# Optimization experiments

Measured on AMD Instinct MI355X. Metric: run time of the kernel, lower is better.

Reference implementation:

```python
import jax, jax.numpy as jnp
import numpy as np

NEG_FILL = -1.0e9
PROB_MIN = 1e-9


def _lstm_cell(x, h, c, w_ih, w_hh, b_ih, b_hh):
    # PyTorch gate order: input, forget, cell(g), output
    gates = x @ w_ih.T + h @ w_hh.T + b_ih + b_hh
    i, f, g, o = jnp.split(gates, 4, axis=-1)
    c_new = jax.nn.sigmoid(f) * c + jax.nn.sigmoid(i) * jnp.tanh(g)
    h_new = jax.nn.sigmoid(o) * jnp.tanh(c_new)
    return h_new, c_new


def setup_inputs() -> dict:
    key = jax.random.key(0)
    B, T, D, H, W = 2048, 100, 128, 256, 256
    ks = jax.random.split(key, 16)
    s_d = 1.0 / np.sqrt(D)
    s_h = 1.0 / np.sqrt(H)
    s_w = 1.0 / np.sqrt(W)
    return {
        "targets": jax.random.normal(ks[0], (B, T, D), jnp.float32),
        "h0": jax.random.normal(ks[1], (1, B, H), jnp.float32),
        "c0": jax.random.normal(ks[2], (1, B, H), jnp.float32),
        "enc_w_ih": jax.random.normal(ks[3], (4 * H, D), jnp.float32) * s_d,
        "enc_w_hh": jax.random.normal(ks[4], (4 * H, H), jnp.float32) * s_h,
        "enc_b_ih": jax.random.normal(ks[5], (4 * H,), jnp.float32) * s_h,
        "enc_b_hh": jax.random.normal(ks[6], (4 * H,), jnp.float32) * s_h,
        "dec_w_ih": jax.random.normal(ks[7], (4 * H, D), jnp.float32) * s_d,
        "dec_w_hh": jax.random.normal(ks[8], (4 * H, H), jnp.float32) * s_h,
        "dec_b_ih": jax.random.normal(ks[9], (4 * H,), jnp.float32) * s_h,
        "dec_b_hh": jax.random.normal(ks[10], (4 * H,), jnp.float32) * s_h,
        "W1": jax.random.normal(ks[11], (W, H), jnp.float32) * s_h,
        "W2": jax.random.normal(ks[12], (W, H), jnp.float32) * s_h,
        "vt": jax.random.normal(ks[13], (W,), jnp.float32) * s_w,
    }


def reference(targets, h0, c0, enc_w_ih, enc_w_hh, enc_b_ih, enc_b_hh,
              dec_w_ih, dec_w_hh, dec_b_ih, dec_b_hh, W1, W2, vt):
    B, T, D = targets.shape
    H = enc_w_hh.shape[1]

    # ---- encoder LSTM (batch_first, zero initial state) ----
    def enc_step(carry, x_t):
        h, c = carry
        h, c = _lstm_cell(x_t, h, c, enc_w_ih, enc_w_hh, enc_b_ih, enc_b_hh)
        return (h, c), h

    z = jnp.zeros((B, H), targets.dtype)
    _, enc_h = jax.lax.scan(enc_step, (z, z), jnp.swapaxes(targets, 0, 1))
    encoder_states = jnp.swapaxes(enc_h, 0, 1)  # [B, T, H]

    blend1 = encoder_states @ W1.T  # [B, T, W]

    a1 = jnp.arange(B)
    init = (h0[0], c0[0], jnp.zeros((B, T), dtype=bool), jnp.zeros_like(targets[:, 0]))

    def dec_step(carry, _):
        h, c, selected, dec_in = carry
        h, c = _lstm_cell(dec_in, h, c, dec_w_ih, dec_w_hh, dec_b_ih, dec_b_hh)
        blend2 = h @ W2.T                                   # [B, W]
        scores = jnp.tanh(blend1 + blend2[:, None, :]) @ vt  # [B, T]
        scores = jnp.where(selected, NEG_FILL, scores)
        sel = jnp.argmax(scores, axis=-1)                    # [B]
        selected = selected.at[a1, sel].set(True)
        probs = jnp.maximum(jax.nn.softmax(scores, axis=-1), PROB_MIN)
        dec_in = targets[a1, sel]                            # [B, D]
        return (h, c, selected, dec_in), probs

    _, probs = jax.lax.scan(dec_step, init, None, length=T)
    return jnp.swapaxes(probs, 0, 1)  # [B, T, T]
```

## Files before the change

### kernel.cpp

```cpp
#include <hip/hip_runtime.h>
#include <math.h>

#define BB   2048
#define TT   100
#define DD   128
#define HH   256
#define NEGF -1.0e9f

__device__ __forceinline__ float sigmoidf_(float x){ return 1.0f/(1.0f+expf(-x)); }

__device__ __forceinline__ float tanh_fast(float x){
  x = fminf(15.f, fmaxf(-15.f, x));
  const float e = __expf(x + x);
  return (e - 1.f) * __builtin_amdgcn_rcpf(e + 1.f);
}

__global__ __launch_bounds__(256) void k_zero_i32(int* __restrict__ p, int n){
  int i = blockIdx.x*256 + threadIdx.x;
  if(i < n) p[i] = 0;
}

__global__ __launch_bounds__(128) void k_gates_cell(
    const float* __restrict__ Xp, int ldx,
    const float* __restrict__ Hp,
    const float* __restrict__ Wih, const float* __restrict__ Whh,
    const float* __restrict__ bih, const float* __restrict__ bhh,
    const float* __restrict__ Cp,
    float* __restrict__ Hout, float* __restrict__ Cout,
    float* __restrict__ Hcopy, int hstride)
{
  __shared__ alignas(16) float Xs[32*68];
  __shared__ alignas(16) float Ws[32*68];
  const int tid = threadIdx.x;
  const int tx = tid & 15;
  const int ty = tid >> 4;
  const int j0 = blockIdx.x * 16;
  const int m0 = blockIdx.y * 64;

  float acc[8][4];
  #pragma unroll
  for(int i=0;i<8;i++)
    #pragma unroll
    for(int s=0;s<4;s++) acc[i][s] = 0.f;

  for(int phase=0; phase<2; phase++){
    const float* Am; int lda; const float* Wm; int ldw; int nt;
    if(phase==0){ if(!Xp) continue; Am=Xp; lda=ldx; Wm=Wih; ldw=DD; nt=4; }
    else        { if(!Hp) continue; Am=Hp; lda=HH;  Wm=Whh; ldw=HH; nt=8; }
    for(int kt=0; kt<nt; kt++){
      const int k0 = kt*32;
      #pragma unroll
      for(int it=0; it<4; it++){
        int q = it*128 + tid; int m = q>>3; int kq = (q&7)<<2;
        const float4 v = *(const float4*)(Am + (size_t)(m0+m)*lda + k0 + kq);
        Xs[(kq+0)*68+m]=v.x; Xs[(kq+1)*68+m]=v.y; Xs[(kq+2)*68+m]=v.z; Xs[(kq+3)*68+m]=v.w;
      }
      #pragma unroll
      for(int it=0; it<4; it++){
        int q = it*128 + tid; int c = q>>3; int kq = (q&7)<<2;
        int n = (c&3)*HH + j0 + (c>>2);
        const float4 v = *(const float4*)(Wm + (size_t)n*ldw + k0 + kq);
        Ws[(kq+0)*68+c]=v.x; Ws[(kq+1)*68+c]=v.y; Ws[(kq+2)*68+c]=v.z; Ws[(kq+3)*68+c]=v.w;
      }
      __syncthreads();
      #pragma unroll
      for(int kk=0; kk<32; kk++){
        const float4 a0 = *(const float4*)&Xs[kk*68 + ty*8];
        const float4 a1 = *(const float4*)&Xs[kk*68 + ty*8 + 4];
        const float4 bv = *(const float4*)&Ws[kk*68 + tx*4];
        const float a[8] = {a0.x,a0.y,a0.z,a0.w,a1.x,a1.y,a1.z,a1.w};
        const float g[4] = {bv.x,bv.y,bv.z,bv.w};
        #pragma unroll
        for(int i=0;i<8;i++)
          #pragma unroll
          for(int s=0;s<4;s++)
            acc[i][s] = fmaf(a[i], g[s], acc[i][s]);
      }
      __syncthreads();
    }
  }

  const int col = j0 + tx;
  const float bi0 = bih[       col] + bhh[       col];
  const float bf0 = bih[  HH + col] + bhh[  HH + col];
  const float bg0 = bih[2*HH + col] + bhh[2*HH + col];
  const float bo0 = bih[3*HH + col] + bhh[3*HH + col];
  #pragma unroll
  for(int i=0;i<8;i++){
    const int b = m0 + ty*8 + i;
    const size_t idx = (size_t)b*HH + col;
    const float iv = acc[i][0] + bi0;
    const float fv = acc[i][1] + bf0;
    const float gv = acc[i][2] + bg0;
    const float ov = acc[i][3] + bo0;
    const float cp = Cp ? Cp[idx] : 0.f;
    const float cn = sigmoidf_(fv)*cp + sigmoidf_(iv)*tanhf(gv);
    const float hn = sigmoidf_(ov)*tanhf(cn);
    Cout[idx] = cn;
    Hout[idx] = hn;
    if(Hcopy) Hcopy[(size_t)b*hstride + col] = hn;
  }
}

__global__ __launch_bounds__(256) void k_gemm_nt(
    const float* __restrict__ A, int lda,
    const float* __restrict__ Bm, int ldb,
    float* __restrict__ C, int ldc, int K)
{
  __shared__ alignas(16) float Xs[32*68];
  __shared__ alignas(16) float Ws[32*68];
  const int tid = threadIdx.x;
  const int tx = tid & 15, ty = tid >> 4;
  const int n0 = blockIdx.x*64, m0 = blockIdx.y*64;
  float acc[4][4];
  #pragma unroll
  for(int i=0;i<4;i++)
    #pragma unroll
    for(int j=0;j<4;j++) acc[i][j]=0.f;

  for(int k0=0; k0<K; k0+=32){
    #pragma unroll
    for(int it=0; it<2; it++){
      int q = it*256 + tid; int m = q>>3; int kq = (q&7)<<2;
      float4 v = *(const float4*)(A + (size_t)(m0+m)*lda + k0 + kq);
      Xs[(kq+0)*68+m]=v.x; Xs[(kq+1)*68+m]=v.y; Xs[(kq+2)*68+m]=v.z; Xs[(kq+3)*68+m]=v.w;
      v = *(const float4*)(Bm + (size_t)(n0+m)*ldb + k0 + kq);
      Ws[(kq+0)*68+m]=v.x; Ws[(kq+1)*68+m]=v.y; Ws[(kq+2)*68+m]=v.z; Ws[(kq+3)*68+m]=v.w;
    }
    __syncthreads();
    #pragma unroll
    for(int kk=0; kk<32; kk++){
      const float4 av = *(const float4*)&Xs[kk*68 + ty*4];
      const float4 bv = *(const float4*)&Ws[kk*68 + tx*4];
      const float a[4] = {av.x,av.y,av.z,av.w};
      const float b[4] = {bv.x,bv.y,bv.z,bv.w};
      #pragma unroll
      for(int i=0;i<4;i++)
        #pragma unroll
        for(int j=0;j<4;j++)
          acc[i][j] = fmaf(a[i], b[j], acc[i][j]);
    }
    __syncthreads();
  }
  #pragma unroll
  for(int i=0;i<4;i++){
    *(float4*)&C[(size_t)(m0+ty*4+i)*ldc + n0 + tx*4] =
        make_float4(acc[i][0],acc[i][1],acc[i][2],acc[i][3]);
  }
}

__global__ __launch_bounds__(256) void k_blend1(float* __restrict__ blend1,
                                                const float* __restrict__ W1)
{
  __shared__ alignas(16) float Af[32*260];
  __shared__ alignas(16) float Ws[32*68];
  const int tid = threadIdx.x;
  const int tx = tid & 15, ty = tid >> 4;
  const size_t r0 = (size_t)blockIdx.x * 32;

  #pragma unroll
  for(int it=0; it<8; it++){
    int q = it*256 + tid; int m = q>>6; int kq = (q&63)<<2;
    *(float4*)&Af[m*260 + kq] = *(const float4*)(blend1 + (r0+m)*256 + kq);
  }
  __syncthreads();

  for(int nc=0; nc<4; nc++){
    const int n0 = nc*64;
    float acc[2][4];
    #pragma unroll
    for(int i=0;i<2;i++)
      #pragma unroll
      for(int j=0;j<4;j++) acc[i][j]=0.f;
    for(int kt=0; kt<8; kt++){
      const int k0 = kt*32;
      __syncthreads();
      #pragma unroll
      for(int it=0; it<2; it++){
        int q = it*256 + tid; int c = q>>3; int kq = (q&7)<<2;
        const float4 v = *(const float4*)(W1 + (size_t)(n0+c)*256 + k0 + kq);
        Ws[(kq+0)*68+c]=v.x; Ws[(kq+1)*68+c]=v.y; Ws[(kq+2)*68+c]=v.z; Ws[(kq+3)*68+c]=v.w;
      }
      __syncthreads();
      #pragma unroll
      for(int kk=0; kk<32; kk++){
        const float4 bv = *(const float4*)&Ws[kk*68 + tx*4];
        const float a0 = Af[(ty*2+0)*260 + k0 + kk];
        const float a1 = Af[(ty*2+1)*260 + k0 + kk];
        acc[0][0]=fmaf(a0,bv.x,acc[0][0]); acc[0][1]=fmaf(a0,bv.y,acc[0][1]);
        acc[0][2]=fmaf(a0,bv.z,acc[0][2]); acc[0][3]=fmaf(a0,bv.w,acc[0][3]);
        acc[1][0]=fmaf(a1,bv.x,acc[1][0]); acc[1][1]=fmaf(a1,bv.y,acc[1][1]);
        acc[1][2]=fmaf(a1,bv.z,acc[1][2]); acc[1][3]=fmaf(a1,bv.w,acc[1][3]);
      }
    }
    #pragma unroll
    for(int i=0;i<2;i++){
      *(float4*)&blend1[(r0 + ty*2 + i)*256 + n0 + tx*4] =
          make_float4(acc[i][0],acc[i][1],acc[i][2],acc[i][3]);
    }
  }
}

__global__ __launch_bounds__(256) void k_scores(
    const float* __restrict__ blend1,
    const float* __restrict__ blend2,
    const float* __restrict__ vt,
    const float* __restrict__ targets,
    int*  __restrict__ selected,
    float* __restrict__ dec_in,
    float* __restrict__ out,
    int s)
{
  __shared__ float vt_s[256], b2_s[256], sc[128];
  __shared__ float M_s, S_s;
  __shared__ int sel_s;
  const int b = blockIdx.x;
  const int tid = threadIdx.x;
  const int lane = tid & 63;
  const int wave = tid >> 6;

  vt_s[tid] = vt[tid];
  b2_s[tid] = blend2[(size_t)b*256 + tid];
  __syncthreads();

  const float4 bb = *(const float4*)&b2_s[lane*4];
  const float4 vv = *(const float4*)&vt_s[lane*4];

  for(int it=0; it<25; it++){
    const int t = wave + it*4;
    const float4 x = *(const float4*)(blend1 + ((size_t)b*TT + t)*256 + lane*4);
    float p;
    p = tanh_fast(x.x + bb.x) * vv.x;
    p = fmaf(tanh_fast(x.y + bb.y), vv.y, p);
    p = fmaf(tanh_fast(x.z + bb.z), vv.z, p);
    p = fmaf(tanh_fast(x.w + bb.w), vv.w, p);
    #pragma unroll
    for(int off=32; off>=1; off>>=1) p += __shfl_xor(p, off, 64);
    if(lane == 0) sc[t] = p;
  }
  __syncthreads();

  if(wave == 0){
    float m1 = selected[(size_t)b*TT + lane] ? NEGF : sc[lane];
    sc[lane] = m1;
    float bestv = m1; int besti = lane;
    float m2 = 0.f;
    const int t2 = lane + 64;
    if(t2 < TT){
      m2 = selected[(size_t)b*TT + t2] ? NEGF : sc[t2];
      sc[t2] = m2;
      if(m2 > bestv){ bestv = m2; besti = t2; }
    }
    #pragma unroll
    for(int off=32; off>=1; off>>=1){
      const float ov = __shfl_xor(bestv, off, 64);
      const int   oi = __shfl_xor(besti, off, 64);
      if(ov > bestv || (ov == bestv && oi < besti)){ bestv = ov; besti = oi; }
    }
    float e = __expf(m1 - bestv);
    if(t2 < TT) e += __expf(m2 - bestv);
    #pragma unroll
    for(int off=32; off>=1; off>>=1) e += __shfl_xor(e, off, 64);
    if(lane == 0){
      M_s = bestv; S_s = e; sel_s = besti;
      selected[(size_t)b*TT + besti] = 1;
    }
  }
  __syncthreads();

  const int sel = sel_s;
  if(tid < TT){
    float p = __expf(sc[tid] - M_s) / S_s;
    out[(size_t)b*TT*TT + (size_t)s*TT + tid] = fmaxf(p, 1e-9f);
  }
  if(tid < DD){
    dec_in[(size_t)b*DD + tid] = targets[((size_t)b*TT + sel)*DD + tid];
  }
}

extern "C" void kernel_launch(void* const* d_in, const int* in_sizes, int n_in,
                              void* d_out, int out_size, void* d_ws, size_t ws_size,
                              hipStream_t stream)
{
  (void)in_sizes; (void)n_in; (void)out_size; (void)ws_size;
  const float* targets  = (const float*)d_in[0];
  const float* h0       = (const float*)d_in[1];
  const float* c0       = (const float*)d_in[2];
  const float* enc_w_ih = (const float*)d_in[3];
  const float* enc_w_hh = (const float*)d_in[4];
  const float* enc_b_ih = (const float*)d_in[5];
  const float* enc_b_hh = (const float*)d_in[6];
  const float* dec_w_ih = (const float*)d_in[7];
  const float* dec_w_hh = (const float*)d_in[8];
  const float* dec_b_ih = (const float*)d_in[9];
  const float* dec_b_hh = (const float*)d_in[10];
  const float* W1       = (const float*)d_in[11];
  const float* W2       = (const float*)d_in[12];
  const float* vt       = (const float*)d_in[13];
  float* out = (float*)d_out;

  float* ws      = (float*)d_ws;
  float* blend1  = ws;
  float* hA      = blend1 + (size_t)BB*TT*256;
  float* hB      = hA + (size_t)BB*HH;
  float* cA      = hB + (size_t)BB*HH;
  float* cB      = cA + (size_t)BB*HH;
  float* blend2  = cB + (size_t)BB*HH;
  float* dec_in  = blend2 + (size_t)BB*HH;
  int*   selected= (int*)(dec_in + (size_t)BB*DD);

  k_zero_i32<<<(BB*TT + 255)/256, 256, 0, stream>>>(selected, BB*TT);

  for(int t=0; t<TT; t++){
    const float* Hp = (t==0) ? nullptr : ((t&1) ? hA : hB);
    const float* Cp = (t==0) ? nullptr : ((t&1) ? cA : cB);
    float* Ho = (t&1) ? hB : hA;
    float* Co = (t&1) ? cB : cA;
    k_gates_cell<<<dim3(16,32), 128, 0, stream>>>(
        targets + (size_t)t*DD, TT*DD,
        Hp, enc_w_ih, enc_w_hh, enc_b_ih, enc_b_hh, Cp,
        Ho, Co, blend1 + (size_t)t*256, TT*256);
  }

  k_blend1<<<BB*TT/32, 256, 0, stream>>>(blend1, W1);

  for(int s=0; s<TT; s++){
    const float* Hp = (s==0) ? h0 : ((s&1) ? hA : hB);
    const float* Cp = (s==0) ? c0 : ((s&1) ? cA : cB);
    float* Ho = (s&1) ? hB : hA;
    float* Co = (s&1) ? cB : cA;
    const float* Xp = (s==0) ? nullptr : dec_in;
    k_gates_cell<<<dim3(16,32), 128, 0, stream>>>(
        Xp, DD, Hp, dec_w_ih, dec_w_hh, dec_b_ih, dec_b_hh, Cp,
        Ho, Co, nullptr, 0);
    k_gemm_nt<<<dim3(4,32), 256, 0, stream>>>(Ho, HH, W2, HH, blend2, HH, HH);
    k_scores<<<BB, 256, 0, stream>>>(blend1, blend2, vt, targets, selected,
                                     dec_in, out, s);
  }
}
```

Baseline: 14.28 ms.

## Fuse blend2 GEMM into scores kernel, one wave per batch row, fast activations

```diff
diff --git a/kernel.cpp b/kernel.cpp
--- a/kernel.cpp
+++ b/kernel.cpp
@@ -7,8 +7,10 @@
 #define HH   256
 #define NEGF -1.0e9f
 
-__device__ __forceinline__ float sigmoidf_(float x){ return 1.0f/(1.0f+expf(-x)); }
-
+__device__ __forceinline__ float sigmoid_fast(float x){
+  const float e = __expf(-x);
+  return __builtin_amdgcn_rcpf(1.f + e);
+}
 __device__ __forceinline__ float tanh_fast(float x){
   x = fminf(15.f, fmaxf(-15.f, x));
   const float e = __expf(x + x);
@@ -94,58 +96,11 @@
     const float gv = acc[i][2] + bg0;
     const float ov = acc[i][3] + bo0;
     const float cp = Cp ? Cp[idx] : 0.f;
-    const float cn = sigmoidf_(fv)*cp + sigmoidf_(iv)*tanhf(gv);
-    const float hn = sigmoidf_(ov)*tanhf(cn);
+    const float cn = sigmoid_fast(fv)*cp + sigmoid_fast(iv)*tanh_fast(gv);
+    const float hn = sigmoid_fast(ov)*tanh_fast(cn);
     Cout[idx] = cn;
     Hout[idx] = hn;
     if(Hcopy) Hcopy[(size_t)b*hstride + col] = hn;
-  }
-}
-
-__global__ __launch_bounds__(256) void k_gemm_nt(
-    const float* __restrict__ A, int lda,
-    const float* __restrict__ Bm, int ldb,
-    float* __restrict__ C, int ldc, int K)
-{
-  __shared__ alignas(16) float Xs[32*68];
-  __shared__ alignas(16) float Ws[32*68];
-  const int tid = threadIdx.x;
-  const int tx = tid & 15, ty = tid >> 4;
-  const int n0 = blockIdx.x*64, m0 = blockIdx.y*64;
-  float acc[4][4];
-  #pragma unroll
-  for(int i=0;i<4;i++)
-    #pragma unroll
-    for(int j=0;j<4;j++) acc[i][j]=0.f;
-
-  for(int k0=0; k0<K; k0+=32){
-    #pragma unroll
-    for(int it=0; it<2; it++){
-      int q = it*256 + tid; int m = q>>3; int kq = (q&7)<<2;
-      float4 v = *(const float4*)(A + (size_t)(m0+m)*lda + k0 + kq);
-      Xs[(kq+0)*68+m]=v.x; Xs[(kq+1)*68+m]=v.y; Xs[(kq+2)*68+m]=v.z; Xs[(kq+3)*68+m]=v.w;
-      v = *(const float4*)(Bm + (size_t)(n0+m)*ldb + k0 + kq);
-      Ws[(kq+0)*68+m]=v.x; Ws[(kq+1)*68+m]=v.y; Ws[(kq+2)*68+m]=v.z; Ws[(kq+3)*68+m]=v.w;
-    }
-    __syncthreads();
-    #pragma unroll
-    for(int kk=0; kk<32; kk++){
-      const float4 av = *(const float4*)&Xs[kk*68 + ty*4];
-      const float4 bv = *(const float4*)&Ws[kk*68 + tx*4];
-      const float a[4] = {av.x,av.y,av.z,av.w};
-      const float b[4] = {bv.x,bv.y,bv.z,bv.w};
-      #pragma unroll
-      for(int i=0;i<4;i++)
-        #pragma unroll
-        for(int j=0;j<4;j++)
-          acc[i][j] = fmaf(a[i], b[j], acc[i][j]);
-    }
-    __syncthreads();
-  }
-  #pragma unroll
-  for(int i=0;i<4;i++){
-    *(float4*)&C[(size_t)(m0+ty*4+i)*ldc + n0 + tx*4] =
-        make_float4(acc[i][0],acc[i][1],acc[i][2],acc[i][3]);
   }
 }
 
@@ -203,7 +158,8 @@
 
 __global__ __launch_bounds__(256) void k_scores(
     const float* __restrict__ blend1,
-    const float* __restrict__ blend2,
+    const float* __restrict__ hcur,
+    const float* __restrict__ W2,
     const float* __restrict__ vt,
     const float* __restrict__ targets,
     int*  __restrict__ selected,
@@ -211,71 +167,87 @@
     float* __restrict__ out,
     int s)
 {
-  __shared__ float vt_s[256], b2_s[256], sc[128];
-  __shared__ float M_s, S_s;
-  __shared__ int sel_s;
-  const int b = blockIdx.x;
-  const int tid = threadIdx.x;
+  __shared__ float h_s[4][256];
+  __shared__ float b2_s[4][256];
+  const int tid  = threadIdx.x;
   const int lane = tid & 63;
   const int wave = tid >> 6;
-
-  vt_s[tid] = vt[tid];
-  b2_s[tid] = blend2[(size_t)b*256 + tid];
+  const int b0   = blockIdx.x * 4;
+
+  #pragma unroll
+  for(int i=0;i<4;i++) h_s[i][tid] = hcur[(size_t)(b0+i)*HH + tid];
   __syncthreads();
 
-  const float4 bb = *(const float4*)&b2_s[lane*4];
-  const float4 vv = *(const float4*)&vt_s[lane*4];
-
-  for(int it=0; it<25; it++){
-    const int t = wave + it*4;
+  {
+    float4 h4[4];
+    #pragma unroll
+    for(int bb=0;bb<4;bb++) h4[bb] = *(const float4*)&h_s[bb][lane*4];
+    for(int j=0;j<64;j++){
+      const int n = wave*64 + j;
+      const float4 w2v = *(const float4*)(W2 + (size_t)n*HH + lane*4);
+      #pragma unroll
+      for(int bb=0;bb<4;bb++){
+        float p = w2v.x*h4[bb].x;
+        p = fmaf(w2v.y, h4[bb].y, p);
+        p = fmaf(w2v.z, h4[bb].z, p);
+        p = fmaf(w2v.w, h4[bb].w, p);
+        #pragma unroll
+        for(int off=32; off>=1; off>>=1) p += __shfl_xor(p, off, 64);
+        if(lane==0) b2_s[bb][n] = p;
+      }
+    }
+  }
+  __syncthreads();
+
+  const int b = b0 + wave;
+  const float4 bb4 = *(const float4*)&b2_s[wave][lane*4];
+  const float4 vv4 = *(const float4*)(vt + lane*4);
+
+  const int t2 = lane + 64;
+  const int sel1 = selected[(size_t)b*TT + lane];
+  const int sel2 = (t2 < TT) ? selected[(size_t)b*TT + t2] : 1;
+
+  float m1 = NEGF, m2 = NEGF;
+  for(int t=0; t<TT; t++){
     const float4 x = *(const float4*)(blend1 + ((size_t)b*TT + t)*256 + lane*4);
     float p;
-    p = tanh_fast(x.x + bb.x) * vv.x;
-    p = fmaf(tanh_fast(x.y + bb.y), vv.y, p);
-    p = fmaf(tanh_fast(x.z + bb.z), vv.z, p);
-    p = fmaf(tanh_fast(x.w + bb.w), vv.w, p);
+    p = tanh_fast(x.x + bb4.x) * vv4.x;
+    p = fmaf(tanh_fast(x.y + bb4.y), vv4.y, p);
+    p = fmaf(tanh_fast(x.z + bb4.z), vv4.z, p);
+    p = fmaf(tanh_fast(x.w + bb4.w), vv4.w, p);
     #pragma unroll
     for(int off=32; off>=1; off>>=1) p += __shfl_xor(p, off, 64);
-    if(lane == 0) sc[t] = p;
-  }
-  __syncthreads();
-
-  if(wave == 0){
-    float m1 = selected[(size_t)b*TT + lane] ? NEGF : sc[lane];
-    sc[lane] = m1;
-    float bestv = m1; int besti = lane;
-    float m2 = 0.f;
-    const int t2 = lane + 64;
-    if(t2 < TT){
-      m2 = selected[(size_t)b*TT + t2] ? NEGF : sc[t2];
-      sc[t2] = m2;
-      if(m2 > bestv){ bestv = m2; besti = t2; }
-    }
-    #pragma unroll
-    for(int off=32; off>=1; off>>=1){
-      const float ov = __shfl_xor(bestv, off, 64);
-      const int   oi = __shfl_xor(besti, off, 64);
-      if(ov > bestv || (ov == bestv && oi < besti)){ bestv = ov; besti = oi; }
-    }
-    float e = __expf(m1 - bestv);
-    if(t2 < TT) e += __expf(m2 - bestv);
-    #pragma unroll
-    for(int off=32; off>=1; off>>=1) e += __shfl_xor(e, off, 64);
-    if(lane == 0){
-      M_s = bestv; S_s = e; sel_s = besti;
-      selected[(size_t)b*TT + besti] = 1;
-    }
-  }
-  __syncthreads();
-
-  const int sel = sel_s;
-  if(tid < TT){
-    float p = __expf(sc[tid] - M_s) / S_s;
-    out[(size_t)b*TT*TT + (size_t)s*TT + tid] = fmaxf(p, 1e-9f);
-  }
-  if(tid < DD){
-    dec_in[(size_t)b*DD + tid] = targets[((size_t)b*TT + sel)*DD + tid];
-  }
+    if(t == lane) m1 = p;
+    if(t == t2)   m2 = p;
+  }
+  if(sel1) m1 = NEGF;
+  if(sel2) m2 = NEGF;
+
+  float bestv = m1; int besti = lane;
+  if(t2 < TT && m2 > bestv){ bestv = m2; besti = t2; }
+  #pragma unroll
+  for(int off=32; off>=1; off>>=1){
+    const float ov = __shfl_xor(bestv, off, 64);
+    const int   oi = __shfl_xor(besti, off, 64);
+    if(ov > bestv || (ov == bestv && oi < besti)){ bestv = ov; besti = oi; }
+  }
+
+  const float e1 = __expf(m1 - bestv);
+  const float e2 = (t2 < TT) ? __expf(m2 - bestv) : 0.f;
+  float S = e1 + e2;
+  #pragma unroll
+  for(int off=32; off>=1; off>>=1) S += __shfl_xor(S, off, 64);
+  const float rS = __builtin_amdgcn_rcpf(S);
+
+  float* orow = out + (size_t)b*TT*TT + (size_t)s*TT;
+  orow[lane] = fmaxf(e1 * rS, 1e-9f);
+  if(t2 < TT) orow[t2] = fmaxf(e2 * rS, 1e-9f);
+
+  if(lane == 0) selected[(size_t)b*TT + besti] = 1;
+
+  const float* trow = targets + ((size_t)b*TT + besti)*DD;
+  dec_in[(size_t)b*DD + lane]      = trow[lane];
+  dec_in[(size_t)b*DD + lane + 64] = trow[lane + 64];
 }
 
 extern "C" void kernel_launch(void* const* d_in, const int* in_sizes, int n_in,
@@ -305,8 +277,7 @@
   float* hB      = hA + (size_t)BB*HH;
   float* cA      = hB + (size_t)BB*HH;
   float* cB      = cA + (size_t)BB*HH;
-  float* blend2  = cB + (size_t)BB*HH;
-  float* dec_in  = blend2 + (size_t)BB*HH;
+  float* dec_in  = cB + (size_t)BB*HH;
   int*   selected= (int*)(dec_in + (size_t)BB*DD);
 
   k_zero_i32<<<(BB*TT + 255)/256, 256, 0, stream>>>(selected, BB*TT);
@@ -333,8 +304,7 @@
     k_gates_cell<<<dim3(16,32), 128, 0, stream>>>(
         Xp, DD, Hp, dec_w_ih, dec_w_hh, dec_b_ih, dec_b_hh, Cp,
         Ho, Co, nullptr, 0);
-    k_gemm_nt<<<dim3(4,32), 256, 0, stream>>>(Ho, HH, W2, HH, blend2, HH, HH);
-    k_scores<<<BB, 256, 0, stream>>>(blend1, blend2, vt, targets, selected,
-                                     dec_in, out, s);
-  }
-}
+    k_scores<<<BB/4, 256, 0, stream>>>(blend1, Ho, W2, vt, targets, selected,
+                                       dec_in, out, s);
+  }
+}
```

Result: slower. 22.40 ms (+56.9%).
